# Optimization experiments

Hardware: AMD Instinct MI355X
Metric: run time of the kernel (lower is better)

## Reference

```python
import jax, jax.numpy as jnp
import numpy as np


def setup_inputs() -> dict:
    key = jax.random.key(0)
    k1, k2, k3 = jax.random.split(key, 3)
    B, S, D_IN, D_OUT, R = 4, 2048, 4096, 4096, 8
    x = jax.random.normal(k1, (B, S, D_IN), dtype=jnp.float32)
    # fixed_linear.weight: [out_features, in_features]
    weight = jax.random.normal(k2, (D_OUT, D_IN), dtype=jnp.float32) * 0.02
    # hra_u: [in_features, r] Householder vectors
    hra_u = jax.random.normal(k3, (D_IN, R), dtype=jnp.float32)
    return {"x": x, "weight": weight, "hra_u": hra_u}


def reference(x, weight, hra_u):
    # Normalize each Householder vector (column) as in the torch module.
    u = hra_u / jnp.linalg.norm(hra_u, axis=0, keepdims=True)  # [in, r]

    # Sequentially apply W <- W (I - 2 u u^T) == W - 2 (W u) u^T  (rank-1 update,
    # mathematically identical to the original's explicit [in,in] GEMM per step).
    def step(w, ui):  # w: [out, in], ui: [in]
        wu = w @ ui                      # [out]
        return w - 2.0 * jnp.outer(wu, ui), None

    new_weight, _ = jax.lax.scan(step, weight, u.T)  # scan over r reflections

    # F.linear(x, new_weight) = x @ new_weight^T, bias=False
    return jnp.einsum("bsd,od->bso", x, new_weight)
```

## Files before the change

### kernel.cpp

```cpp
#include <hip/hip_runtime.h>
#include <hip/hip_bf16.h>


#define D_IN   4096
#define D_OUT  4096
#define R_HH   8
#define M_ROWS 8192

typedef short bf16x8 __attribute__((ext_vector_type(8)));
typedef float f32x4  __attribute__((ext_vector_type(4)));

__device__ inline unsigned short f2bf(float f) {
    unsigned int x = __float_as_uint(f);
    unsigned int lsb = (x >> 16) & 1u;
    x += 0x7fffu + lsb;
    return (unsigned short)(x >> 16);
}

__device__ inline void async16(const unsigned short* g, char* l) {
    __builtin_amdgcn_global_load_lds(
        (const __attribute__((address_space(1))) void*)g,
        (__attribute__((address_space(3))) void*)l,
        16, 0, 0);
}

__global__ __launch_bounds__(1024) void prep(const float* __restrict__ hu,
                                             float* __restrict__ G,
                                             float* __restrict__ inv8) {
    float d[36];
    #pragma unroll
    for (int p = 0; p < 36; p++) d[p] = 0.f;
    for (int r = threadIdx.x; r < D_IN; r += 1024) {
        const float4* h4 = (const float4*)&hu[r * R_HH];
        float4 a = h4[0], b = h4[1];
        float h[8] = {a.x, a.y, a.z, a.w, b.x, b.y, b.z, b.w};
        int p = 0;
        #pragma unroll
        for (int i = 0; i < 8; i++)
            #pragma unroll
            for (int j = i; j < 8; j++)
                d[p++] += h[i] * h[j];
    }
    #pragma unroll
    for (int p = 0; p < 36; p++)
        #pragma unroll
        for (int off = 32; off > 0; off >>= 1)
            d[p] += __shfl_down(d[p], off, 64);
    __shared__ float red[16 * 36];
    const int wave = threadIdx.x >> 6, lane = threadIdx.x & 63;
    if (lane == 0)
        #pragma unroll
        for (int p = 0; p < 36; p++) red[wave * 36 + p] = d[p];
    __syncthreads();
    __shared__ float dd[36];
    if (threadIdx.x < 36) {
        float s = 0.f;
        #pragma unroll
        for (int w = 0; w < 16; w++) s += red[w * 36 + threadIdx.x];
        dd[threadIdx.x] = s;
    }
    __syncthreads();
    auto idx = [](int a, int b) { return a * 8 + b - (a * (a + 1)) / 2; };
    if (threadIdx.x < 64) {
        const int i = threadIdx.x >> 3, j = threadIdx.x & 7;
        const int a = i < j ? i : j, b = i < j ? j : i;
        const float gi = rsqrtf(dd[idx(i, i)]);
        const float gj = rsqrtf(dd[idx(j, j)]);
        G[threadIdx.x] = dd[idx(a, b)] * gi * gj;
        if (j == 0) inv8[i] = gi;
    }
}

__global__ void wu_gemv(const float* __restrict__ W, const float* __restrict__ hu,
                        const float* __restrict__ inv8, float* __restrict__ Y) {
    const int o = blockIdx.x;
    const float* wrow = W + (size_t)o * D_IN;
    float acc[8] = {0,0,0,0,0,0,0,0};
    for (int k = threadIdx.x; k < D_IN; k += 256) {
        float w = wrow[k];
        const float4* u4 = (const float4*)&hu[k * R_HH];
        float4 a = u4[0], b = u4[1];
        acc[0] += w * a.x; acc[1] += w * a.y; acc[2] += w * a.z; acc[3] += w * a.w;
        acc[4] += w * b.x; acc[5] += w * b.y; acc[6] += w * b.z; acc[7] += w * b.w;
    }
    __shared__ float red[8 * 256];
    #pragma unroll
    for (int j = 0; j < 8; j++) red[j * 256 + threadIdx.x] = acc[j];
    __syncthreads();
    for (int off = 128; off > 0; off >>= 1) {
        if (threadIdx.x < off)
            #pragma unroll
            for (int j = 0; j < 8; j++)
                red[j * 256 + threadIdx.x] += red[j * 256 + threadIdx.x + off];
        __syncthreads();
    }
    if (threadIdx.x < 8)
        Y[(size_t)o * R_HH + threadIdx.x] = red[threadIdx.x * 256] * inv8[threadIdx.x];
}

__global__ void vcalc(const float* __restrict__ Y, const float* __restrict__ G,
                      float* __restrict__ V) {
    const int o = blockIdx.x * 256 + threadIdx.x;
    __shared__ float g[64];
    if (threadIdx.x < 64) g[threadIdx.x] = G[threadIdx.x];
    __syncthreads();
    float y[8], v[8];
    const float4* y4 = (const float4*)&Y[(size_t)o * R_HH];
    float4 a = y4[0], b = y4[1];
    y[0]=a.x; y[1]=a.y; y[2]=a.z; y[3]=a.w; y[4]=b.x; y[5]=b.y; y[6]=b.z; y[7]=b.w;
    #pragma unroll
    for (int i = 0; i < 8; i++) {
        float t = y[i];
        #pragma unroll
        for (int j = 0; j < 8; j++)
            if (j < i) t -= 2.0f * g[j * 8 + i] * v[j];
        v[i] = t;
    }
    float4* v4 = (float4*)&V[(size_t)o * R_HH];
    v4[0] = make_float4(v[0], v[1], v[2], v[3]);
    v4[1] = make_float4(v[4], v[5], v[6], v[7]);
}

__global__ void wn_cast(const float* __restrict__ W, const float* __restrict__ hu,
                        const float* __restrict__ inv8, const float* __restrict__ V,
                        unsigned short* __restrict__ Wn) {
    const int o = blockIdx.x;
    __shared__ float vs[8];
    if (threadIdx.x < 8)
        vs[threadIdx.x] = V[(size_t)o * R_HH + threadIdx.x] * inv8[threadIdx.x];
    __syncthreads();
    float v[8];
    #pragma unroll
    for (int i = 0; i < 8; i++) v[i] = vs[i];
    const float4* wrow = (const float4*)(W + (size_t)o * D_IN);
    ushort4* wnrow = (ushort4*)(Wn + (size_t)o * D_IN);
    for (int k4 = threadIdx.x; k4 < D_IN / 4; k4 += 256) {
        float4 wv = wrow[k4];
        float wa[4] = {wv.x, wv.y, wv.z, wv.w};
        float out[4];
        #pragma unroll
        for (int e = 0; e < 4; e++) {
            const int k = k4 * 4 + e;
            const float4* u4 = (const float4*)&hu[k * R_HH];
            float4 ua = u4[0], ub = u4[1];
            float corr = v[0]*ua.x + v[1]*ua.y + v[2]*ua.z + v[3]*ua.w
                       + v[4]*ub.x + v[5]*ub.y + v[6]*ub.z + v[7]*ub.w;
            out[e] = wa[e] - 2.0f * corr;
        }
        ushort4 r;
        r.x = f2bf(out[0]); r.y = f2bf(out[1]); r.z = f2bf(out[2]); r.w = f2bf(out[3]);
        wnrow[k4] = r;
    }
}

__global__ void cast_x(const float4* __restrict__ x, ushort4* __restrict__ xb, int n4) {
    const int g = blockIdx.x * 256 + threadIdx.x;
    if (g >= n4) return;
    float4 f = x[g];
    ushort4 r;
    r.x = f2bf(f.x); r.y = f2bf(f.y); r.z = f2bf(f.z); r.w = f2bf(f.w);
    xb[g] = r;
}

__global__ __launch_bounds__(512, 2) void gemm256(
    const unsigned short* __restrict__ A,
    const unsigned short* __restrict__ B,
    float* __restrict__ C) {
    constexpr int K  = D_IN;
    constexpr int NN = D_OUT;
    constexpr int NT = K / 64;

    extern __shared__ __align__(16) char lds[];

    const int tid  = threadIdx.x;
    const int lane = tid & 63;
    const int wave = tid >> 6;

    const int bid = blockIdx.x;
    const int cpx = gridDim.x >> 3;
    const int swz = (bid & 7) * cpx + (bid >> 3);
    const int TN  = NN / 256;
    const int tm  = swz / TN, tn = swz - tm * TN;

    const size_t rA0 = (size_t)tm * 256;
    const size_t rB0 = (size_t)tn * 256;

    const int wr = (wave >> 2) * 128;
    const int wc = (wave & 3) * 64;

    const int sRow = tid >> 2;
    const int sCol = ((tid & 3) * 8) ^ ((sRow & 8) ? 16 : 0);
    const unsigned short* gA = A + (rA0 + sRow) * (size_t)K + sCol;
    const unsigned short* gB = B + (rB0 + sRow) * (size_t)K + sCol;

    auto stageA = [&](int kt, int h) {
        const unsigned short* g = gA + (size_t)(h * 128) * K + kt * 64;
        char* l = lds + (kt & 1) * 32768 + h * 8192 + tid * 16;
        async16(g, l);
        async16(g + 32, l + 16384);
    };
    auto stageB = [&](int kt, int h) {
        const unsigned short* g = gB + (size_t)(h * 128) * K + kt * 64;
        char* l = lds + 65536 + (kt & 1) * 32768 + h * 8192 + tid * 16;
        async16(g, l);
        async16(g + 32, l + 16384);
    };

    const int kb   = ((lane >> 4) * 16) ^ ((lane & 8) ? 32 : 0);
    const int rdA0 = (wr + (lane & 15)) * 64 + kb;
    const int rdB0 = 65536 + (wc + (lane & 15)) * 64 + kb;

    auto LDA = [&](int bb, int i, int s) -> bf16x8 {
        return *(const bf16x8*)(lds + bb * 32768 + s * 16384 + i * 1024 + rdA0);
    };
    auto LDB = [&](int bb, int j, int s) -> bf16x8 {
        return *(const bf16x8*)(lds + bb * 32768 + s * 16384 + j * 1024 + rdB0);
    };

    f32x4 acc[8][4];
    #pragma unroll
    for (int i = 0; i < 8; i++)
        #pragma unroll
        for (int j = 0; j < 4; j++)
            acc[i][j] = (f32x4){0.f, 0.f, 0.f, 0.f};

    stageA(0, 0); stageA(0, 1); stageB(0, 0); stageB(0, 1);
    stageB(1, 0); stageB(1, 1);
    asm volatile("s_waitcnt vmcnt(4)" ::: "memory");
    __builtin_amdgcn_s_barrier();

    #pragma unroll 2
    for (int kt = 0; kt < NT; ++kt) {
        const int bb = kt & 1;

        bf16x8 a0[4][2], a1[4][2], b[4][2];
        #pragma unroll
        for (int i = 0; i < 4; i++) { a0[i][0] = LDA(bb, i, 0); a0[i][1] = LDA(bb, i, 1); }
        #pragma unroll
        for (int j = 0; j < 4; j++) { b[j][0] = LDB(bb, j, 0); b[j][1] = LDB(bb, j, 1); }
        if (kt + 1 < NT) stageA(kt + 1, 0);
        __builtin_amdgcn_s_setprio(1);
        #pragma unroll
        for (int i = 0; i < 4; i++)
            #pragma unroll
            for (int j = 0; j < 2; j++) {
                acc[i][j] = __builtin_amdgcn_mfma_f32_16x16x32_bf16(a0[i][0], b[j][0], acc[i][j], 0, 0, 0);
                acc[i][j] = __builtin_amdgcn_mfma_f32_16x16x32_bf16(a0[i][1], b[j][1], acc[i][j], 0, 0, 0);
            }
        __builtin_amdgcn_s_setprio(0);
        if (kt + 1 < NT) stageA(kt + 1, 1);
        __builtin_amdgcn_s_setprio(1);
        #pragma unroll
        for (int i = 0; i < 4; i++)
            #pragma unroll
            for (int j = 2; j < 4; j++) {
                acc[i][j] = __builtin_amdgcn_mfma_f32_16x16x32_bf16(a0[i][0], b[j][0], acc[i][j], 0, 0, 0);
                acc[i][j] = __builtin_amdgcn_mfma_f32_16x16x32_bf16(a0[i][1], b[j][1], acc[i][j], 0, 0, 0);
            }
        __builtin_amdgcn_s_setprio(0);
        #pragma unroll
        for (int i = 0; i < 4; i++) { a1[i][0] = LDA(bb, 4 + i, 0); a1[i][1] = LDA(bb, 4 + i, 1); }

        asm volatile("" ::: "memory");
        __builtin_amdgcn_s_barrier();
        asm volatile("" ::: "memory");

        if (kt + 2 < NT) stageB(kt + 2, 0);
        __builtin_amdgcn_s_setprio(1);
        #pragma unroll
        for (int i = 0; i < 4; i++)
            #pragma unroll
            for (int j = 0; j < 2; j++) {
                acc[4 + i][j] = __builtin_amdgcn_mfma_f32_16x16x32_bf16(a1[i][0], b[j][0], acc[4 + i][j], 0, 0, 0);
                acc[4 + i][j] = __builtin_amdgcn_mfma_f32_16x16x32_bf16(a1[i][1], b[j][1], acc[4 + i][j], 0, 0, 0);
            }
        __builtin_amdgcn_s_setprio(0);
        if (kt + 2 < NT) stageB(kt + 2, 1);
        __builtin_amdgcn_s_setprio(1);
        #pragma unroll
        for (int i = 0; i < 4; i++)
            #pragma unroll
            for (int j = 2; j < 4; j++) {
                acc[4 + i][j] = __builtin_amdgcn_mfma_f32_16x16x32_bf16(a1[i][0], b[j][0], acc[4 + i][j], 0, 0, 0);
                acc[4 + i][j] = __builtin_amdgcn_mfma_f32_16x16x32_bf16(a1[i][1], b[j][1], acc[4 + i][j], 0, 0, 0);
            }
        __builtin_amdgcn_s_setprio(0);

        if (kt < NT - 2)
            asm volatile("s_waitcnt vmcnt(4)" ::: "memory");
        else
            asm volatile("s_waitcnt vmcnt(0)" ::: "memory");
        __builtin_amdgcn_s_barrier();
    }

    const int crow = (lane >> 4) * 4;
    const int ccol = lane & 15;
    #pragma unroll
    for (int i = 0; i < 8; i++) {
        #pragma unroll
        for (int j = 0; j < 4; j++) {
            size_t base = (rA0 + wr + i * 16 + crow) * (size_t)NN
                        + (rB0 + wc + j * 16 + ccol);
            #pragma unroll
            for (int r = 0; r < 4; r++)
                C[base + (size_t)r * NN] = acc[i][j][r];
        }
    }
}

extern "C" void kernel_launch(void* const* d_in, const int* in_sizes, int n_in,
                              void* d_out, int out_size, void* d_ws, size_t ws_size,
                              hipStream_t stream) {
    const float* x      = (const float*)d_in[0];
    const float* weight = (const float*)d_in[1];
    const float* hra_u  = (const float*)d_in[2];
    float* out = (float*)d_out;

    char* w = (char*)d_ws;
    unsigned short* Xb = (unsigned short*)w;
    unsigned short* Wn = (unsigned short*)(w + (size_t)64 * 1024 * 1024);
    float* Y   = (float*)(w + (size_t)96 * 1024 * 1024);
    float* V   = Y + (size_t)D_IN * R_HH;
    float* G   = V + (size_t)D_IN * R_HH;
    float* inv = G + 64;

    static int attr_done = 0;
    if (!attr_done) {
        hipFuncSetAttribute((const void*)gemm256,
                            hipFuncAttributeMaxDynamicSharedMemorySize, 131072);
        attr_done = 1;
    }

    prep<<<1, 1024, 0, stream>>>(hra_u, G, inv);
    wu_gemv<<<D_OUT, 256, 0, stream>>>(weight, hra_u, inv, Y);
    vcalc<<<D_OUT / 256, 256, 0, stream>>>(Y, G, V);
    wn_cast<<<D_OUT, 256, 0, stream>>>(weight, hra_u, inv, V, Wn);

    const int n4 = M_ROWS * D_IN / 4;
    cast_x<<<(n4 + 255) / 256, 256, 0, stream>>>((const float4*)x, (ushort4*)Xb, n4);

    gemm256<<<dim3((M_ROWS / 256) * (D_OUT / 256)), 512, 131072, stream>>>(Xb, Wn, out);
}
```

Before: 570.2 us.

## Switch GEMM to 32x32x16 MFMA, fuse vcalc into wn_cast, grid-stride cast_x

The main GEMM now uses 32x32x16 bf16 MFMA tiles with f32x16 accumulators in place of 16x16x32. The LDS read addressing and the output store pattern change to match the new layout. This cuts the number of MFMA issues and LDS fragment reads per k-step. Separately, the small vcalc kernel is folded into wn_cast, which removes one launch and the V buffer, and cast_x becomes a fixed-size grid-stride loop.

```diff
diff --git a/kernel.cpp b/kernel.cpp
--- a/kernel.cpp
+++ b/kernel.cpp
@@ -7,8 +7,9 @@
 #define R_HH   8
 #define M_ROWS 8192
 
-typedef short bf16x8 __attribute__((ext_vector_type(8)));
-typedef float f32x4  __attribute__((ext_vector_type(4)));
+typedef short bf16x8  __attribute__((ext_vector_type(8)));
+typedef float f32x4   __attribute__((ext_vector_type(4)));
+typedef float f32x16  __attribute__((ext_vector_type(16)));
 
 __device__ inline unsigned short f2bf(float f) {
     unsigned int x = __float_as_uint(f);
@@ -98,40 +99,28 @@
         Y[(size_t)o * R_HH + threadIdx.x] = red[threadIdx.x * 256] * inv8[threadIdx.x];
 }
 
-__global__ void vcalc(const float* __restrict__ Y, const float* __restrict__ G,
-                      float* __restrict__ V) {
-    const int o = blockIdx.x * 256 + threadIdx.x;
-    __shared__ float g[64];
-    if (threadIdx.x < 64) g[threadIdx.x] = G[threadIdx.x];
-    __syncthreads();
-    float y[8], v[8];
-    const float4* y4 = (const float4*)&Y[(size_t)o * R_HH];
-    float4 a = y4[0], b = y4[1];
-    y[0]=a.x; y[1]=a.y; y[2]=a.z; y[3]=a.w; y[4]=b.x; y[5]=b.y; y[6]=b.z; y[7]=b.w;
-    #pragma unroll
-    for (int i = 0; i < 8; i++) {
-        float t = y[i];
-        #pragma unroll
-        for (int j = 0; j < 8; j++)
-            if (j < i) t -= 2.0f * g[j * 8 + i] * v[j];
-        v[i] = t;
-    }
-    float4* v4 = (float4*)&V[(size_t)o * R_HH];
-    v4[0] = make_float4(v[0], v[1], v[2], v[3]);
-    v4[1] = make_float4(v[4], v[5], v[6], v[7]);
-}
-
 __global__ void wn_cast(const float* __restrict__ W, const float* __restrict__ hu,
-                        const float* __restrict__ inv8, const float* __restrict__ V,
-                        unsigned short* __restrict__ Wn) {
+                        const float* __restrict__ inv8, const float* __restrict__ Y,
+                        const float* __restrict__ G, unsigned short* __restrict__ Wn) {
     const int o = blockIdx.x;
-    __shared__ float vs[8];
-    if (threadIdx.x < 8)
-        vs[threadIdx.x] = V[(size_t)o * R_HH + threadIdx.x] * inv8[threadIdx.x];
+    __shared__ float gs[64];
+    __shared__ float ys[8];
+    __shared__ float is[8];
+    if (threadIdx.x < 64) gs[threadIdx.x] = G[threadIdx.x];
+    else if (threadIdx.x < 72) ys[threadIdx.x - 64] = Y[(size_t)o * R_HH + threadIdx.x - 64];
+    else if (threadIdx.x < 80) is[threadIdx.x - 72] = inv8[threadIdx.x - 72];
     __syncthreads();
     float v[8];
     #pragma unroll
-    for (int i = 0; i < 8; i++) v[i] = vs[i];
+    for (int i = 0; i < 8; i++) {
+        float t = ys[i];
+        #pragma unroll
+        for (int j = 0; j < 8; j++)
+            if (j < i) t -= 2.0f * gs[j * 8 + i] * v[j];
+        v[i] = t;
+    }
+    #pragma unroll
+    for (int i = 0; i < 8; i++) v[i] *= is[i];
     const float4* wrow = (const float4*)(W + (size_t)o * D_IN);
     ushort4* wnrow = (ushort4*)(Wn + (size_t)o * D_IN);
     for (int k4 = threadIdx.x; k4 < D_IN / 4; k4 += 256) {
@@ -154,12 +143,12 @@
 }
 
 __global__ void cast_x(const float4* __restrict__ x, ushort4* __restrict__ xb, int n4) {
-    const int g = blockIdx.x * 256 + threadIdx.x;
-    if (g >= n4) return;
-    float4 f = x[g];
-    ushort4 r;
-    r.x = f2bf(f.x); r.y = f2bf(f.y); r.z = f2bf(f.z); r.w = f2bf(f.w);
-    xb[g] = r;
+    for (int g = blockIdx.x * 256 + threadIdx.x; g < n4; g += gridDim.x * 256) {
+        float4 f = x[g];
+        ushort4 r;
+        r.x = f2bf(f.x); r.y = f2bf(f.y); r.z = f2bf(f.z); r.w = f2bf(f.w);
+        xb[g] = r;
+    }
 }
 
 __global__ __launch_bounds__(512, 2) void gemm256(
@@ -206,23 +195,27 @@
         async16(g + 32, l + 16384);
     };
 
-    const int kb   = ((lane >> 4) * 16) ^ ((lane & 8) ? 32 : 0);
-    const int rdA0 = (wr + (lane & 15)) * 64 + kb;
-    const int rdB0 = 65536 + (wc + (lane & 15)) * 64 + kb;
+    const int xorv = (lane & 8) ? 32 : 0;
+    const int k16  = (lane >> 5) * 16;
+    const int rbA  = (wr + (lane & 31)) * 64;
+    const int rbB  = (wc + (lane & 31)) * 64;
 
     auto LDA = [&](int bb, int i, int s) -> bf16x8 {
-        return *(const bf16x8*)(lds + bb * 32768 + s * 16384 + i * 1024 + rdA0);
+        return *(const bf16x8*)(lds + bb * 32768 + (s >> 1) * 16384
+                                + i * 2048 + rbA + (((s & 1) * 32 + k16) ^ xorv));
     };
     auto LDB = [&](int bb, int j, int s) -> bf16x8 {
-        return *(const bf16x8*)(lds + bb * 32768 + s * 16384 + j * 1024 + rdB0);
+        return *(const bf16x8*)(lds + 65536 + bb * 32768 + (s >> 1) * 16384
+                                + j * 2048 + rbB + (((s & 1) * 32 + k16) ^ xorv));
     };
 
-    f32x4 acc[8][4];
-    #pragma unroll
-    for (int i = 0; i < 8; i++)
-        #pragma unroll
-        for (int j = 0; j < 4; j++)
-            acc[i][j] = (f32x4){0.f, 0.f, 0.f, 0.f};
+    f32x16 acc[4][2];
+    #pragma unroll
+    for (int i = 0; i < 4; i++)
+        #pragma unroll
+        for (int j = 0; j < 2; j++)
+            acc[i][j] = (f32x16){0.f,0.f,0.f,0.f,0.f,0.f,0.f,0.f,
+                                 0.f,0.f,0.f,0.f,0.f,0.f,0.f,0.f};
 
     stageA(0, 0); stageA(0, 1); stageB(0, 0); stageB(0, 1);
     stageB(1, 0); stageB(1, 1);
@@ -233,57 +226,63 @@
     for (int kt = 0; kt < NT; ++kt) {
         const int bb = kt & 1;
 
-        bf16x8 a0[4][2], a1[4][2], b[4][2];
-        #pragma unroll
-        for (int i = 0; i < 4; i++) { a0[i][0] = LDA(bb, i, 0); a0[i][1] = LDA(bb, i, 1); }
-        #pragma unroll
-        for (int j = 0; j < 4; j++) { b[j][0] = LDB(bb, j, 0); b[j][1] = LDB(bb, j, 1); }
+        bf16x8 a[2][4], b[2][4];
+        #pragma unroll
+        for (int i = 0; i < 2; i++)
+            #pragma unroll
+            for (int s = 0; s < 4; s++) a[i][s] = LDA(bb, i, s);
+        #pragma unroll
+        for (int j = 0; j < 2; j++)
+            #pragma unroll
+            for (int s = 0; s < 4; s++) b[j][s] = LDB(bb, j, s);
         if (kt + 1 < NT) stageA(kt + 1, 0);
         __builtin_amdgcn_s_setprio(1);
         #pragma unroll
-        for (int i = 0; i < 4; i++)
-            #pragma unroll
-            for (int j = 0; j < 2; j++) {
-                acc[i][j] = __builtin_amdgcn_mfma_f32_16x16x32_bf16(a0[i][0], b[j][0], acc[i][j], 0, 0, 0);
-                acc[i][j] = __builtin_amdgcn_mfma_f32_16x16x32_bf16(a0[i][1], b[j][1], acc[i][j], 0, 0, 0);
-            }
+        for (int s = 0; s < 2; s++)
+            #pragma unroll
+            for (int i = 0; i < 2; i++)
+                #pragma unroll
+                for (int j = 0; j < 2; j++)
+                    acc[i][j] = __builtin_amdgcn_mfma_f32_32x32x16_bf16(a[i][s], b[j][s], acc[i][j], 0, 0, 0);
         __builtin_amdgcn_s_setprio(0);
         if (kt + 1 < NT) stageA(kt + 1, 1);
         __builtin_amdgcn_s_setprio(1);
         #pragma unroll
-        for (int i = 0; i < 4; i++)
-            #pragma unroll
-            for (int j = 2; j < 4; j++) {
-                acc[i][j] = __builtin_amdgcn_mfma_f32_16x16x32_bf16(a0[i][0], b[j][0], acc[i][j], 0, 0, 0);
-                acc[i][j] = __builtin_amdgcn_mfma_f32_16x16x32_bf16(a0[i][1], b[j][1], acc[i][j], 0, 0, 0);
-            }
+        for (int s = 2; s < 4; s++)
+            #pragma unroll
+            for (int i = 0; i < 2; i++)
+                #pragma unroll
+                for (int j = 0; j < 2; j++)
+                    acc[i][j] = __builtin_amdgcn_mfma_f32_32x32x16_bf16(a[i][s], b[j][s], acc[i][j], 0, 0, 0);
         __builtin_amdgcn_s_setprio(0);
-        #pragma unroll
-        for (int i = 0; i < 4; i++) { a1[i][0] = LDA(bb, 4 + i, 0); a1[i][1] = LDA(bb, 4 + i, 1); }
 
         asm volatile("" ::: "memory");
         __builtin_amdgcn_s_barrier();
         asm volatile("" ::: "memory");
 
+        #pragma unroll
+        for (int i = 0; i < 2; i++)
+            #pragma unroll
+            for (int s = 0; s < 4; s++) a[i][s] = LDA(bb, 2 + i, s);
         if (kt + 2 < NT) stageB(kt + 2, 0);
         __builtin_amdgcn_s_setprio(1);
         #pragma unroll
-        for (int i = 0; i < 4; i++)
-            #pragma unroll
-            for (int j = 0; j < 2; j++) {
-                acc[4 + i][j] = __builtin_amdgcn_mfma_f32_16x16x32_bf16(a1[i][0], b[j][0], acc[4 + i][j], 0, 0, 0);
-                acc[4 + i][j] = __builtin_amdgcn_mfma_f32_16x16x32_bf16(a1[i][1], b[j][1], acc[4 + i][j], 0, 0, 0);
-            }
+        for (int s = 0; s < 2; s++)
+            #pragma unroll
+            for (int i = 0; i < 2; i++)
+                #pragma unroll
+                for (int j = 0; j < 2; j++)
+                    acc[2 + i][j] = __builtin_amdgcn_mfma_f32_32x32x16_bf16(a[i][s], b[j][s], acc[2 + i][j], 0, 0, 0);
         __builtin_amdgcn_s_setprio(0);
         if (kt + 2 < NT) stageB(kt + 2, 1);
         __builtin_amdgcn_s_setprio(1);
         #pragma unroll
-        for (int i = 0; i < 4; i++)
-            #pragma unroll
-            for (int j = 2; j < 4; j++) {
-                acc[4 + i][j] = __builtin_amdgcn_mfma_f32_16x16x32_bf16(a1[i][0], b[j][0], acc[4 + i][j], 0, 0, 0);
-                acc[4 + i][j] = __builtin_amdgcn_mfma_f32_16x16x32_bf16(a1[i][1], b[j][1], acc[4 + i][j], 0, 0, 0);
-            }
+        for (int s = 2; s < 4; s++)
+            #pragma unroll
+            for (int i = 0; i < 2; i++)
+                #pragma unroll
+                for (int j = 0; j < 2; j++)
+                    acc[2 + i][j] = __builtin_amdgcn_mfma_f32_32x32x16_bf16(a[i][s], b[j][s], acc[2 + i][j], 0, 0, 0);
         __builtin_amdgcn_s_setprio(0);
 
         if (kt < NT - 2)
@@ -293,17 +292,19 @@
         __builtin_amdgcn_s_barrier();
     }
 
-    const int crow = (lane >> 4) * 4;
-    const int ccol = lane & 15;
-    #pragma unroll
-    for (int i = 0; i < 8; i++) {
-        #pragma unroll
-        for (int j = 0; j < 4; j++) {
-            size_t base = (rA0 + wr + i * 16 + crow) * (size_t)NN
-                        + (rB0 + wc + j * 16 + ccol);
-            #pragma unroll
-            for (int r = 0; r < 4; r++)
-                C[base + (size_t)r * NN] = acc[i][j][r];
+    const int ccol = lane & 31;
+    const int rsub = 4 * (lane >> 5);
+    #pragma unroll
+    for (int i = 0; i < 4; i++) {
+        #pragma unroll
+        for (int j = 0; j < 2; j++) {
+            size_t base = (rA0 + wr + i * 32 + rsub) * (size_t)NN
+                        + (rB0 + wc + j * 32 + ccol);
+            #pragma unroll
+            for (int r = 0; r < 16; r++) {
+                const int row = (r & 3) + 8 * (r >> 2);
+                C[base + (size_t)row * NN] = acc[i][j][r];
+            }
         }
     }
 }
@@ -320,8 +321,7 @@
     unsigned short* Xb = (unsigned short*)w;
     unsigned short* Wn = (unsigned short*)(w + (size_t)64 * 1024 * 1024);
     float* Y   = (float*)(w + (size_t)96 * 1024 * 1024);
-    float* V   = Y + (size_t)D_IN * R_HH;
-    float* G   = V + (size_t)D_IN * R_HH;
+    float* G   = Y + (size_t)D_IN * R_HH;
     float* inv = G + 64;
 
     static int attr_done = 0;
@@ -333,11 +333,10 @@
 
     prep<<<1, 1024, 0, stream>>>(hra_u, G, inv);
     wu_gemv<<<D_OUT, 256, 0, stream>>>(weight, hra_u, inv, Y);
-    vcalc<<<D_OUT / 256, 256, 0, stream>>>(Y, G, V);
-    wn_cast<<<D_OUT, 256, 0, stream>>>(weight, hra_u, inv, V, Wn);
+    wn_cast<<<D_OUT, 256, 0, stream>>>(weight, hra_u, inv, Y, G, Wn);
 
     const int n4 = M_ROWS * D_IN / 4;
-    cast_x<<<(n4 + 255) / 256, 256, 0, stream>>>((const float4*)x, (ushort4*)Xb, n4);
+    cast_x<<<4096, 256, 0, stream>>>((const float4*)x, (ushort4*)Xb, n4);
 
     gemm256<<<dim3((M_ROWS / 256) * (D_OUT / 256)), 512, 131072, stream>>>(Xb, Wn, out);
 }
```

Measured after the change: 612.3 us. 1.07x slower.
